# Performance work log

Measured on AMD Instinct MI355X. Metric: run time of the kernel, lower is better.

Reference implementation:

```python
import jax, jax.numpy as jnp
import numpy as np

ETA = 1.0
C_STAB = 0.1
SIGMA2 = 512.0  # RBF bandwidth, kernel_args['sigma2']
N_SAMPLE, S, D = 8192, 64, 512


def rbf_kernel(x, sigma2):
    # K[i,j] = exp(-||x_i - x_j||^2 / (2*sigma2)); x: [n, d] -> K: [n, n]
    sq = jnp.sum(x * x, axis=1)
    d2 = sq[:, None] + sq[None, :] - 2.0 * (x @ x.T)
    return jnp.exp(-d2 / (2.0 * sigma2))


def setup_inputs() -> dict:
    key = jax.random.key(0)
    k1, k2, k3 = jax.random.split(key, 3)
    return {
        "input_data": jax.random.normal(k1, (N_SAMPLE, D), dtype=jnp.float32),
        "weight": jax.random.normal(k2, (N_SAMPLE, S), dtype=jnp.float32),
        "inv_lambda_diag": jax.random.normal(k3, (S,), dtype=jnp.float32),
    }


def reference(input_data, weight, inv_lambda_diag):
    K = rbf_kernel(input_data, SIGMA2)          # [n, n]
    E = weight.T @ K                             # [s, n] : e_j for all samples at once
    # loss1 = sum_i e_i^T diag(inv_lambda) e_i, scaled
    loss1 = -jnp.sum(inv_lambda_diag[:, None] * E * E) / (2.0 * ETA ** 2)
    # loss2 = trace(W^T K W) = sum_{s,n} E[s,n] * W[n,s]
    loss2 = jnp.einsum("sn,ns->", E, weight) / (2.0 * ETA)
    L = loss1 + loss2
    return L + (C_STAB / 2.0) * jnp.square(L)
```

## Files before the change

### kernel.cpp

```cpp
#include <hip/hip_runtime.h>
#include <hip/hip_bf16.h>

typedef __bf16 bf16x8 __attribute__((ext_vector_type(8)));
typedef float f32x4 __attribute__((ext_vector_type(4)));
typedef long longx2 __attribute__((ext_vector_type(2)));

#define N 8192
#define D 512
#define NS 64

#define XS_OFF 0
#define WT_OFF (4 * 1024 * 1024)
#define SQ_OFF (WT_OFF + 1024 * 1024)
#define EP_OFF (SQ_OFF + 32 * 1024)
#define SC_OFF (EP_OFF + 8 * 64 * 8192 * 4)

__global__ __launch_bounds__(256) void prep(const float* __restrict__ X,
                                            const float* __restrict__ W,
                                            unsigned char* __restrict__ Xs,
                                            float* __restrict__ sq,
                                            __bf16* __restrict__ WTs,
                                            float* __restrict__ Sacc) {
    __shared__ float T[64][65];
    int t = threadIdx.x;
    if (blockIdx.x == 0 && t == 0) {
        Sacc[0] = 0.f; Sacc[1] = 0.f; ((int*)Sacc)[2] = 0;
    }
    if (blockIdx.x < 2048) {
        int row = blockIdx.x * 4 + (t >> 6);
        int l = t & 63;
        const float* src = X + (size_t)row * D + l * 8;
        float4 v0 = *(const float4*)src;
        float4 v1 = *(const float4*)(src + 4);
        int w0 = __builtin_amdgcn_cvt_pk_fp8_f32(v0.x, v0.y, 0, false);
        w0     = __builtin_amdgcn_cvt_pk_fp8_f32(v0.z, v0.w, w0, true);
        int w1 = __builtin_amdgcn_cvt_pk_fp8_f32(v1.x, v1.y, 0, false);
        w1     = __builtin_amdgcn_cvt_pk_fp8_f32(v1.z, v1.w, w1, true);
        int g = l >> 3, kh = (l >> 2) & 1, q = l & 3;
        int pos = g * 64 + q * 16 + kh * 8;
        uint2 pk = make_uint2((unsigned)w0, (unsigned)w1);
        *(uint2*)(Xs + (size_t)row * 512 + pos) = pk;
        float acc = v0.x*v0.x + v0.y*v0.y + v0.z*v0.z + v0.w*v0.w
                  + v1.x*v1.x + v1.y*v1.y + v1.z*v1.z + v1.w*v1.w;
        for (int off = 32; off > 0; off >>= 1) acc += __shfl_down(acc, off);
        if (l == 0) sq[row] = acc;
    } else {
        int i0 = (blockIdx.x - 2048) * 64;
        for (int j = 0; j < 16; ++j) {
            int idx = t + 256 * j;
            T[idx & 63][idx >> 6] = W[(size_t)(i0 + (idx >> 6)) * NS + (idx & 63)];
        }
        __syncthreads();
        for (int h = 0; h < 2; ++h)
            for (int j = 0; j < 8; ++j) {
                int idx = t + 256 * j;
                int s = idx >> 5, il = idx & 31;
                WTs[(size_t)((i0 >> 5) + h) * 2048 + idx] = (__bf16)T[s][h * 32 + il];
            }
    }
}

__global__ __launch_bounds__(256, 2) void kpca_main(
        const unsigned char* __restrict__ Xs, const __bf16* __restrict__ WTs,
        const float* __restrict__ sq, float* __restrict__ Ep) {
    __shared__ __align__(16) unsigned char Xi[2][8192];
    __shared__ __align__(16) unsigned char XnHi[128 * 272];
    __shared__ __align__(16) __bf16 KT[128 * 72];

    const int t = threadIdx.x;
    const int w = t >> 6, l = t & 63;
    const int quad = l >> 4, l15 = l & 15;
    const int wm = w >> 1, wn = w & 1;
    const int n0 = blockIdx.x * 128;
    const int ic0 = blockIdx.y * 1024;

    longx2 bc[4][4];
    {
        const unsigned char* Bb = Xs + (size_t)(n0 + wn * 64 + l15) * 512 + quad * 16;
        #pragma unroll
        for (int k8 = 0; k8 < 4; ++k8)
            #pragma unroll
            for (int nt = 0; nt < 4; ++nt)
                bc[k8][nt] = *(const longx2*)(Bb + nt * (16 * 512) + k8 * 64);
    }
    {
        int r = t >> 1, h = t & 1;
        const unsigned char* g = Xs + (size_t)(n0 + r) * 512 + 256 + h * 128;
        unsigned char* d = XnHi + r * 272 + h * 128;
        #pragma unroll
        for (int j = 0; j < 8; ++j)
            *(uint4*)(d + j * 16) = *(const uint4*)(g + j * 16);
    }
    float sqn_v[4];
    for (int nt = 0; nt < 4; ++nt)
        sqn_v[nt] = sq[n0 + wn * 64 + nt * 16 + l15];

    f32x4 accE[4][2];
    for (int st = 0; st < 4; ++st)
        for (int n2 = 0; n2 < 2; ++n2)
            accE[st][n2] = (f32x4){0.f, 0.f, 0.f, 0.f};

    const int ra = t >> 2, blk = (t & 3) * 16;

    {
        const unsigned char* g = Xs + (size_t)(ic0 + ra) * 512 + blk;
        *(uint4*)(Xi[0] + t * 16)        = *(const uint4*)g;
        *(uint4*)(Xi[0] + t * 16 + 4096) = *(const uint4*)(g + 64 * 512);
    }

    for (int it = 0; it < 8; ++it) {
        const int i0 = ic0 + it * 128;
        f32x4 accG[4][4];
        for (int mt = 0; mt < 4; ++mt)
            for (int nt = 0; nt < 4; ++nt)
                accG[mt][nt] = (f32x4){0.f, 0.f, 0.f, 0.f};

        #pragma unroll
        for (int kc8 = 0; kc8 < 8; ++kc8) {
            uint4 qA, qB;
            const bool stage = (kc8 < 7) || (it < 7);
            if (stage) {
                const int kn = (kc8 + 1) & 7;
                const int i0n = i0 + ((kc8 == 7) ? 128 : 0);
                const unsigned char* g = Xs + (size_t)(i0n + ra) * 512 + kn * 64 + blk;
                qA = *(const uint4*)g;
                qB = *(const uint4*)(g + 64 * 512);
            }
            __syncthreads();
            const unsigned char* xb = Xi[kc8 & 1];
            longx2 a[4], b[4];
            #pragma unroll
            for (int mt = 0; mt < 4; ++mt)
                a[mt] = *(const longx2*)(xb + (wm * 64 + mt * 16 + l15) * 64 + quad * 16);
            if (kc8 < 4) {
                #pragma unroll
                for (int nt = 0; nt < 4; ++nt) b[nt] = bc[kc8][nt];
            } else {
                #pragma unroll
                for (int nt = 0; nt < 4; ++nt)
                    b[nt] = *(const longx2*)(XnHi + (wn * 64 + nt * 16 + l15) * 272 +
                                             (kc8 - 4) * 64 + quad * 16);
            }
            #pragma unroll
            for (int mt = 0; mt < 4; ++mt)
                #pragma unroll
                for (int nt = 0; nt < 4; ++nt)
                    accG[mt][nt] = __builtin_amdgcn_mfma_f32_16x16x32_fp8_fp8(
                        a[mt][0], b[nt][0], accG[mt][nt], 0, 0, 0);
            #pragma unroll
            for (int mt = 0; mt < 4; ++mt)
                #pragma unroll
                for (int nt = 0; nt < 4; ++nt)
                    accG[mt][nt] = __builtin_amdgcn_mfma_f32_16x16x32_fp8_fp8(
                        a[mt][1], b[nt][1], accG[mt][nt], 0, 0, 0);
            if (stage) {
                unsigned char* xd = Xi[(kc8 + 1) & 1];
                *(uint4*)(xd + t * 16)        = qA;
                *(uint4*)(xd + t * 16 + 4096) = qB;
            }
        }

        uint2 pk[4][4];
        #pragma unroll
        for (int mt = 0; mt < 4; ++mt) {
            f32x4 si = *(const f32x4*)(sq + i0 + wm * 64 + mt * 16 + quad * 4);
            #pragma unroll
            for (int nt = 0; nt < 4; ++nt) {
                float sn = sqn_v[nt];
                union { __bf16 h[4]; uint2 u; } u;
                #pragma unroll
                for (int r = 0; r < 4; ++r) {
                    float d2 = si[r] + sn - 2.0f * accG[mt][nt][r];
                    u.h[r] = (__bf16)__expf(d2 * -9.765625e-4f);
                }
                pk[mt][nt] = u.u;
            }
        }

        const __bf16* wslab = WTs + (size_t)(i0 >> 5) * 2048;
        bf16x8 aw[2][4];
        #pragma unroll
        for (int kc2 = 0; kc2 < 2; ++kc2)
            for (int st = 0; st < 4; ++st)
                aw[kc2][st] = *(const bf16x8*)(wslab + kc2 * 2048 +
                                               (st * 16 + l15) * 32 + quad * 8);

        __syncthreads();
        if (wm == 0) {
            #pragma unroll
            for (int mt = 0; mt < 4; ++mt)
                for (int nt = 0; nt < 4; ++nt)
                    *(uint2*)(KT + (wn * 64 + nt * 16 + l15) * 72 + mt * 16 + quad * 4)
                        = pk[mt][nt];
        }
        __syncthreads();
        #pragma unroll
        for (int kc2 = 0; kc2 < 2; ++kc2) {
            bf16x8 bk[2];
            for (int n2 = 0; n2 < 2; ++n2)
                bk[n2] = *(const bf16x8*)(KT + (w * 32 + n2 * 16 + l15) * 72 +
                                          kc2 * 32 + quad * 8);
            #pragma unroll
            for (int st = 0; st < 4; ++st)
                for (int n2 = 0; n2 < 2; ++n2)
                    accE[st][n2] = __builtin_amdgcn_mfma_f32_16x16x32_bf16(
                        aw[kc2][st], bk[n2], accE[st][n2], 0, 0, 0);
        }
        #pragma unroll
        for (int kc2 = 0; kc2 < 2; ++kc2)
            for (int st = 0; st < 4; ++st)
                aw[kc2][st] = *(const bf16x8*)(wslab + (kc2 + 2) * 2048 +
                                               (st * 16 + l15) * 32 + quad * 8);
        __syncthreads();
        if (wm == 1) {
            #pragma unroll
            for (int mt = 0; mt < 4; ++mt)
                for (int nt = 0; nt < 4; ++nt)
                    *(uint2*)(KT + (wn * 64 + nt * 16 + l15) * 72 + mt * 16 + quad * 4)
                        = pk[mt][nt];
        }
        __syncthreads();
        #pragma unroll
        for (int kc2 = 0; kc2 < 2; ++kc2) {
            bf16x8 bk[2];
            for (int n2 = 0; n2 < 2; ++n2)
                bk[n2] = *(const bf16x8*)(KT + (w * 32 + n2 * 16 + l15) * 72 +
                                          kc2 * 32 + quad * 8);
            #pragma unroll
            for (int st = 0; st < 4; ++st)
                for (int n2 = 0; n2 < 2; ++n2)
                    accE[st][n2] = __builtin_amdgcn_mfma_f32_16x16x32_bf16(
                        aw[kc2][st], bk[n2], accE[st][n2], 0, 0, 0);
        }
    }

    float* ep = Ep + (size_t)blockIdx.y * (NS * N);
    #pragma unroll
    for (int st = 0; st < 4; ++st)
        for (int n2 = 0; n2 < 2; ++n2)
            for (int r = 0; r < 4; ++r) {
                int s = st * 16 + quad * 4 + r;
                int n = n0 + w * 32 + n2 * 16 + l15;
                ep[(size_t)s * N + n] = accE[st][n2][r];
            }
}

__global__ __launch_bounds__(256) void loss_kernel(const float* __restrict__ Ep,
                                                   const __bf16* __restrict__ WTs,
                                                   const float* __restrict__ lam,
                                                   float* __restrict__ Sacc,
                                                   float* __restrict__ out) {
    int s = blockIdx.x >> 2;
    int nb = (blockIdx.x & 3) * 2048;
    int t = threadIdx.x;
    float a1 = 0.f, a2 = 0.f;
    for (int j = 0; j < 8; ++j) {
        int n = nb + t + j * 256;
        float e = 0.f;
        #pragma unroll
        for (int c = 0; c < 8; ++c)
            e += Ep[(size_t)c * (NS * N) + (size_t)s * N + n];
        a1 += e * e;
        a2 += e * (float)WTs[(size_t)(n >> 5) * 2048 + s * 32 + (n & 31)];
    }
    for (int off = 32; off > 0; off >>= 1) {
        a1 += __shfl_down(a1, off);
        a2 += __shfl_down(a2, off);
    }
    __shared__ float r1[4], r2[4];
    int wv = t >> 6, ln = t & 63;
    if (ln == 0) { r1[wv] = a1; r2[wv] = a2; }
    __syncthreads();
    if (t == 0) {
        atomicAdd(Sacc + 0, lam[s] * (r1[0] + r1[1] + r1[2] + r1[3]));
        atomicAdd(Sacc + 1, r2[0] + r2[1] + r2[2] + r2[3]);
        __threadfence();
        int prev = atomicAdd((int*)Sacc + 2, 1);
        if (prev == 255) {
            __threadfence();
            volatile float* vs = (volatile float*)Sacc;
            float L = 0.5f * (vs[1] - vs[0]);
            out[0] = L + 0.05f * L * L;
        }
    }
}

extern "C" void kernel_launch(void* const* d_in, const int* in_sizes, int n_in,
                              void* d_out, int out_size, void* d_ws, size_t ws_size,
                              hipStream_t stream) {
    const float* X   = (const float*)d_in[0];
    const float* W   = (const float*)d_in[1];
    const float* lam = (const float*)d_in[2];
    float* out = (float*)d_out;
    char* ws = (char*)d_ws;
    unsigned char* Xs = (unsigned char*)(ws + XS_OFF);
    __bf16* WTs = (__bf16*)(ws + WT_OFF);
    float* sq   = (float*)(ws + SQ_OFF);
    float* Ep   = (float*)(ws + EP_OFF);
    float* Sacc = (float*)(ws + SC_OFF);

    prep<<<2048 + 128, 256, 0, stream>>>(X, W, Xs, sq, WTs, Sacc);
    kpca_main<<<dim3(64, 8), 256, 0, stream>>>(Xs, WTs, sq, Ep);
    loss_kernel<<<256, 256, 0, stream>>>(Ep, WTs, lam, Sacc, out);
}
```

Baseline: 146.5 us.

## Switch Gram GEMM to scaled 16x16x128 FP8 MFMA with swizzled single-buffer LDS

Replaces the 16x16x32 FP8 MFMAs in the Gram-matrix stage with the gfx950 scaled 16x16x128 f8f6f4 MFMA, using unit scales. The input layout becomes plain row-major and the K loop runs in 128-wide steps. The i-tile now sits in a single XOR-swizzled LDS buffer that is aliased with the KT buffer, with register prefetch plus explicit barriers, and the matmul section is wrapped in s_setprio. The aim is fewer MFMA issues and fewer LDS bank conflicts, at the cost of extra barriers per step and the loss of double buffering.

New measurement: 214.5 us. +46.4%, slower.

```diff
diff --git a/kernel.cpp b/kernel.cpp
--- a/kernel.cpp
+++ b/kernel.cpp
@@ -4,6 +4,7 @@
 typedef __bf16 bf16x8 __attribute__((ext_vector_type(8)));
 typedef float f32x4 __attribute__((ext_vector_type(4)));
 typedef long longx2 __attribute__((ext_vector_type(2)));
+typedef int i32x8 __attribute__((ext_vector_type(8)));
 
 #define N 8192
 #define D 512
@@ -14,6 +15,9 @@
 #define SQ_OFF (WT_OFF + 1024 * 1024)
 #define EP_OFF (SQ_OFF + 32 * 1024)
 #define SC_OFF (EP_OFF + 8 * 64 * 8192 * 4)
+
+#define BAR() do { asm volatile("s_waitcnt lgkmcnt(0)" ::: "memory"); \
+                   __builtin_amdgcn_s_barrier(); } while (0)
 
 __global__ __launch_bounds__(256) void prep(const float* __restrict__ X,
                                             const float* __restrict__ W,
@@ -36,10 +40,8 @@
         w0     = __builtin_amdgcn_cvt_pk_fp8_f32(v0.z, v0.w, w0, true);
         int w1 = __builtin_amdgcn_cvt_pk_fp8_f32(v1.x, v1.y, 0, false);
         w1     = __builtin_amdgcn_cvt_pk_fp8_f32(v1.z, v1.w, w1, true);
-        int g = l >> 3, kh = (l >> 2) & 1, q = l & 3;
-        int pos = g * 64 + q * 16 + kh * 8;
         uint2 pk = make_uint2((unsigned)w0, (unsigned)w1);
-        *(uint2*)(Xs + (size_t)row * 512 + pos) = pk;
+        *(uint2*)(Xs + (size_t)row * 512 + l * 8) = pk;
         float acc = v0.x*v0.x + v0.y*v0.y + v0.z*v0.z + v0.w*v0.w
                   + v1.x*v1.x + v1.y*v1.y + v1.z*v1.z + v1.w*v1.w;
         for (int off = 32; off > 0; off >>= 1) acc += __shfl_down(acc, off);
@@ -63,9 +65,10 @@
 __global__ __launch_bounds__(256, 2) void kpca_main(
         const unsigned char* __restrict__ Xs, const __bf16* __restrict__ WTs,
         const float* __restrict__ sq, float* __restrict__ Ep) {
-    __shared__ __align__(16) unsigned char Xi[2][8192];
-    __shared__ __align__(16) unsigned char XnHi[128 * 272];
-    __shared__ __align__(16) __bf16 KT[128 * 72];
+    __shared__ __align__(16) unsigned char XiKT[18432];
+    __shared__ __align__(16) unsigned char XnHi[128 * 400];
+    unsigned char* Xi = XiKT;
+    __bf16* KT = (__bf16*)XiKT;
 
     const int t = threadIdx.x;
     const int w = t >> 6, l = t & 63;
@@ -74,89 +77,118 @@
     const int n0 = blockIdx.x * 128;
     const int ic0 = blockIdx.y * 1024;
 
-    longx2 bc[4][4];
+    union U8 { longx2 h[2]; i32x8 v; };
+
+    U8 bc[4];
     {
-        const unsigned char* Bb = Xs + (size_t)(n0 + wn * 64 + l15) * 512 + quad * 16;
-        #pragma unroll
-        for (int k8 = 0; k8 < 4; ++k8)
-            #pragma unroll
-            for (int nt = 0; nt < 4; ++nt)
-                bc[k8][nt] = *(const longx2*)(Bb + nt * (16 * 512) + k8 * 64);
+        const unsigned char* Bb = Xs + (size_t)(n0 + wn * 64 + l15) * 512 + quad * 32;
+        #pragma unroll
+        for (int nt = 0; nt < 4; ++nt) {
+            bc[nt].h[0] = *(const longx2*)(Bb + nt * 8192);
+            bc[nt].h[1] = *(const longx2*)(Bb + nt * 8192 + 16);
+        }
     }
     {
         int r = t >> 1, h = t & 1;
-        const unsigned char* g = Xs + (size_t)(n0 + r) * 512 + 256 + h * 128;
-        unsigned char* d = XnHi + r * 272 + h * 128;
-        #pragma unroll
-        for (int j = 0; j < 8; ++j)
+        const unsigned char* g = Xs + (size_t)(n0 + r) * 512 + 128 + h * 192;
+        unsigned char* d = XnHi + r * 400 + h * 192;
+        #pragma unroll
+        for (int j = 0; j < 12; ++j)
             *(uint4*)(d + j * 16) = *(const uint4*)(g + j * 16);
     }
     float sqn_v[4];
+    #pragma unroll
     for (int nt = 0; nt < 4; ++nt)
         sqn_v[nt] = sq[n0 + wn * 64 + nt * 16 + l15];
 
     f32x4 accE[4][2];
+    #pragma unroll
     for (int st = 0; st < 4; ++st)
         for (int n2 = 0; n2 < 2; ++n2)
             accE[st][n2] = (f32x4){0.f, 0.f, 0.f, 0.f};
 
-    const int ra = t >> 2, blk = (t & 3) * 16;
+    const int rB = t >> 3;
+    const int cB = (t & 7) * 16;
+    const int swoff = (((t & 7) ^ ((t >> 3) & 7)) << 4);
+
+    const int oswL = (((2 * quad)     ^ (l15 & 7)) << 4);
+    const int oswH = (((2 * quad + 1) ^ (l15 & 7)) << 4);
 
     {
-        const unsigned char* g = Xs + (size_t)(ic0 + ra) * 512 + blk;
-        *(uint4*)(Xi[0] + t * 16)        = *(const uint4*)g;
-        *(uint4*)(Xi[0] + t * 16 + 4096) = *(const uint4*)(g + 64 * 512);
-    }
+        const unsigned char* g = Xs + (size_t)(ic0 + rB) * 512 + cB;
+        #pragma unroll
+        for (int j = 0; j < 4; ++j)
+            *(uint4*)(Xi + (size_t)(j * 32 + rB) * 128 + swoff) =
+                *(const uint4*)(g + (size_t)j * 32 * 512);
+    }
+
+    uint4 q[4];
 
     for (int it = 0; it < 8; ++it) {
         const int i0 = ic0 + it * 128;
         f32x4 accG[4][4];
+        #pragma unroll
         for (int mt = 0; mt < 4; ++mt)
             for (int nt = 0; nt < 4; ++nt)
                 accG[mt][nt] = (f32x4){0.f, 0.f, 0.f, 0.f};
 
-        #pragma unroll
-        for (int kc8 = 0; kc8 < 8; ++kc8) {
-            uint4 qA, qB;
-            const bool stage = (kc8 < 7) || (it < 7);
+        if (it > 0) {
+            BAR();
+            #pragma unroll
+            for (int j = 0; j < 4; ++j)
+                *(uint4*)(Xi + (size_t)(j * 32 + rB) * 128 + swoff) = q[j];
+        }
+
+        #pragma unroll
+        for (int ks = 0; ks < 4; ++ks) {
+            const bool stage = (ks < 3) || (it < 7);
             if (stage) {
-                const int kn = (kc8 + 1) & 7;
-                const int i0n = i0 + ((kc8 == 7) ? 128 : 0);
-                const unsigned char* g = Xs + (size_t)(i0n + ra) * 512 + kn * 64 + blk;
-                qA = *(const uint4*)g;
-                qB = *(const uint4*)(g + 64 * 512);
-            }
-            __syncthreads();
-            const unsigned char* xb = Xi[kc8 & 1];
-            longx2 a[4], b[4];
+                const int itn = (ks < 3) ? it : it + 1;
+                const int ksn = (ks < 3) ? ks + 1 : 0;
+                const unsigned char* g =
+                    Xs + (size_t)(ic0 + itn * 128 + rB) * 512 + ksn * 128 + cB;
+                #pragma unroll
+                for (int j = 0; j < 4; ++j)
+                    q[j] = *(const uint4*)(g + (size_t)j * 32 * 512);
+            }
+            BAR();
+
+            U8 a[4], bb[4];
+            const unsigned char* abase = Xi + (wm * 64 + l15) * 128;
+            #pragma unroll
+            for (int mt = 0; mt < 4; ++mt) {
+                a[mt].h[0] = *(const longx2*)(abase + mt * 2048 + oswL);
+                a[mt].h[1] = *(const longx2*)(abase + mt * 2048 + oswH);
+            }
+            if (ks == 0) {
+                #pragma unroll
+                for (int nt = 0; nt < 4; ++nt) bb[nt] = bc[nt];
+            } else {
+                const unsigned char* bbase =
+                    XnHi + (wn * 64 + l15) * 400 + (ks - 1) * 128 + quad * 32;
+                #pragma unroll
+                for (int nt = 0; nt < 4; ++nt) {
+                    bb[nt].h[0] = *(const longx2*)(bbase + nt * 6400);
+                    bb[nt].h[1] = *(const longx2*)(bbase + nt * 6400 + 16);
+                }
+            }
+            __builtin_amdgcn_s_setprio(1);
             #pragma unroll
             for (int mt = 0; mt < 4; ++mt)
-                a[mt] = *(const longx2*)(xb + (wm * 64 + mt * 16 + l15) * 64 + quad * 16);
-            if (kc8 < 4) {
-                #pragma unroll
-                for (int nt = 0; nt < 4; ++nt) b[nt] = bc[kc8][nt];
-            } else {
                 #pragma unroll
                 for (int nt = 0; nt < 4; ++nt)
-                    b[nt] = *(const longx2*)(XnHi + (wn * 64 + nt * 16 + l15) * 272 +
-                                             (kc8 - 4) * 64 + quad * 16);
-            }
-            #pragma unroll
-            for (int mt = 0; mt < 4; ++mt)
-                #pragma unroll
-                for (int nt = 0; nt < 4; ++nt)
-                    accG[mt][nt] = __builtin_amdgcn_mfma_f32_16x16x32_fp8_fp8(
-                        a[mt][0], b[nt][0], accG[mt][nt], 0, 0, 0);
-            #pragma unroll
-            for (int mt = 0; mt < 4; ++mt)
-                #pragma unroll
-                for (int nt = 0; nt < 4; ++nt)
-                    accG[mt][nt] = __builtin_amdgcn_mfma_f32_16x16x32_fp8_fp8(
-                        a[mt][1], b[nt][1], accG[mt][nt], 0, 0, 0);
-            if (stage) {
-                unsigned char* xd = Xi[(kc8 + 1) & 1];
-                *(uint4*)(xd + t * 16)        = qA;
-                *(uint4*)(xd + t * 16 + 4096) = qB;
+                    accG[mt][nt] = __builtin_amdgcn_mfma_scale_f32_16x16x128_f8f6f4(
+                        a[mt].v, bb[nt].v, accG[mt][nt],
+                        0, 0,
+                        0, 0x7F7F7F7F,
+                        0, 0x7F7F7F7F);
+            __builtin_amdgcn_s_setprio(0);
+
+            if (ks < 3) {
+                BAR();
+                #pragma unroll
+                for (int j = 0; j < 4; ++j)
+                    *(uint4*)(Xi + (size_t)(j * 32 + rB) * 128 + swoff) = q[j];
             }
         }
 
@@ -185,7 +217,7 @@
                 aw[kc2][st] = *(const bf16x8*)(wslab + kc2 * 2048 +
                                                (st * 16 + l15) * 32 + quad * 8);
 
-        __syncthreads();
+        BAR();
         if (wm == 0) {
             #pragma unroll
             for (int mt = 0; mt < 4; ++mt)
@@ -193,7 +225,7 @@
                     *(uint2*)(KT + (wn * 64 + nt * 16 + l15) * 72 + mt * 16 + quad * 4)
                         = pk[mt][nt];
         }
-        __syncthreads();
+        BAR();
         #pragma unroll
         for (int kc2 = 0; kc2 < 2; ++kc2) {
             bf16x8 bk[2];
@@ -211,7 +243,7 @@
             for (int st = 0; st < 4; ++st)
                 aw[kc2][st] = *(const bf16x8*)(wslab + (kc2 + 2) * 2048 +
                                                (st * 16 + l15) * 32 + quad * 8);
-        __syncthreads();
+        BAR();
         if (wm == 1) {
             #pragma unroll
             for (int mt = 0; mt < 4; ++mt)
@@ -219,7 +251,7 @@
                     *(uint2*)(KT + (wn * 64 + nt * 16 + l15) * 72 + mt * 16 + quad * 4)
                         = pk[mt][nt];
         }
-        __syncthreads();
+        BAR();
         #pragma unroll
         for (int kc2 = 0; kc2 < 2; ++kc2) {
             bf16x8 bk[2];
```
